# Optimization experiments

Hardware: AMD Instinct MI355X
Metric: run time of the kernel (lower is better)

Reference implementation:

```python
import jax, jax.numpy as jnp
import numpy as np
from jax import lax

DIM = 1024
BATCH = 16
WIDTH = 2048
DECAY = 0.99


def setup_inputs() -> dict:
    key = jax.random.key(0)
    k1, k2, k3, k4 = jax.random.split(key, 4)
    scale = 1.0 / np.sqrt(DIM)
    x = jax.random.normal(k1, (BATCH, WIDTH, DIM), dtype=jnp.float32)
    state = jnp.zeros((BATCH, DIM), dtype=jnp.float32)
    Wv = jax.random.normal(k2, (DIM, DIM), dtype=jnp.float32) * scale
    Wr = jax.random.normal(k3, (DIM, DIM), dtype=jnp.float32) * scale
    Wc = jax.random.normal(k4, (DIM, DIM), dtype=jnp.float32) * scale
    return {"x": x, "state": state, "Wv": Wv, "Wr": Wr, "Wc": Wc}


def reference(x, state, Wv, Wr, Wc):
    # x: [B, W, D], state: [B, D]; fixed-decay RWKV recurrence along width.
    decay = jnp.asarray(DECAY, dtype=x.dtype)
    one_minus = jnp.asarray(1.0, dtype=x.dtype) - decay
    v = jnp.einsum('bwd,de->bwe', x, Wv)                 # value projection
    r = jax.nn.sigmoid(jnp.einsum('bwd,de->bwe', x, Wr))  # receptance

    # scan over width (time) axis: elems shaped [W, B, D]
    def step(s_prev, inp):
        v_t, r_t, x_t = inp
        s_curr = decay * s_prev + one_minus * v_t
        y_t = x_t + r_t * s_curr
        return s_curr, y_t

    elems = (jnp.swapaxes(v, 0, 1), jnp.swapaxes(r, 0, 1), jnp.swapaxes(x, 0, 1))
    new_state, y_t = lax.scan(step, state, elems)
    y = jnp.swapaxes(y_t, 0, 1)                          # [B, W, D]
    y = y + jnp.einsum('bwd,de->bwe', y, Wc)             # minimal channel mix
    return y, new_state
```

## Files before the change

kernel.cpp:

```cpp
#include <hip/hip_runtime.h>
#include <hip/hip_bf16.h>
#include <math.h>


#define MROWS 32768
#define NCHUNK 16
#define CHUNKL 128
#define DECAY_F 0.99f
#define OM_F 0.01f

typedef __attribute__((ext_vector_type(8))) short short8;
typedef __attribute__((ext_vector_type(4))) float floatx4;

using bf16 = __hip_bfloat16;
using bf162 = __hip_bfloat162;

__device__ __forceinline__ void async_copy16(const void* g, void* l) {
  __builtin_amdgcn_global_load_lds(
      (const __attribute__((address_space(1))) unsigned int*)g,
      (__attribute__((address_space(3))) unsigned int*)l, 16, 0, 0);
}

#define S_BARRIER() asm volatile("s_barrier" ::: "memory")
#define VMCNT3()                                                               \
  do {                                                                         \
    asm volatile("s_waitcnt vmcnt(3)" ::: "memory");                           \
    __builtin_amdgcn_sched_barrier(0);                                         \
  } while (0)
#define VMCNT0()                                                               \
  do {                                                                         \
    asm volatile("s_waitcnt vmcnt(0)" ::: "memory");                           \
    __builtin_amdgcn_sched_barrier(0);                                         \
  } while (0)

__global__ void prep_x(const float* __restrict__ X, bf16* __restrict__ Xb) {
  const int idx = blockIdx.x * 256 + threadIdx.x;
  const float4 v = ((const float4*)X)[idx];
  union { ushort4 u; bf16 h[4]; } pk;
  pk.h[0] = __float2bfloat16(v.x);
  pk.h[1] = __float2bfloat16(v.y);
  pk.h[2] = __float2bfloat16(v.z);
  pk.h[3] = __float2bfloat16(v.w);
  ((ushort4*)Xb)[idx] = pk.u;
}

__global__ void prep_weights(const float* __restrict__ Wv,
                             const float* __restrict__ Wr,
                             const float* __restrict__ Wc,
                             bf16* __restrict__ WT) {
  __shared__ float tile[32][33];
  const int bk = blockIdx.x * 32;
  const int bn = blockIdx.y * 32;
  const float* src;
  int nbase = bn;
  if (bn < 1024)      { src = Wv; }
  else if (bn < 2048) { src = Wr; nbase = bn - 1024; }
  else                { src = Wc; nbase = bn - 2048; }
  const int tx = threadIdx.x;
  const int ty = threadIdx.y;
  #pragma unroll
  for (int i = ty; i < 32; i += 8)
    tile[i][tx] = src[(size_t)(bk + i) * 1024 + nbase + tx];
  __syncthreads();
  #pragma unroll
  for (int i = ty; i < 32; i += 8)
    WT[(size_t)(bn + i) * 1024 + bk + tx] = __float2bfloat16(tile[tx][i]);
}

#define PH_MFMA(M0)                                                            \
  __builtin_amdgcn_s_setprio(1);                                               \
  _Pragma("unroll")                                                            \
  for (int nf = 0; nf < 4; ++nf)                                               \
    acc[M0][nf] = __builtin_amdgcn_mfma_f32_16x16x32_bf16(                     \
        fa[M0], fb[nf], acc[M0][nf], 0, 0, 0);                                 \
  _Pragma("unroll")                                                            \
  for (int nf = 0; nf < 4; ++nf)                                               \
    acc[M0 + 1][nf] = __builtin_amdgcn_mfma_f32_16x16x32_bf16(                 \
        fa[M0 + 1], fb[nf], acc[M0 + 1][nf], 0, 0, 0);                         \
  __builtin_amdgcn_s_setprio(0);

#define MFMA_ALL()                                                             \
  __builtin_amdgcn_s_setprio(1);                                               \
  _Pragma("unroll")                                                            \
  for (int mf = 0; mf < 8; ++mf)                                               \
    _Pragma("unroll")                                                          \
    for (int nf = 0; nf < 4; ++nf)                                             \
      acc[mf][nf] = __builtin_amdgcn_mfma_f32_16x16x32_bf16(                   \
          fa[mf], fb[nf], acc[mf][nf], 0, 0, 0);                               \
  __builtin_amdgcn_s_setprio(0);

template <int MODE>
__global__ __launch_bounds__(512, 2) void gemm8(const bf16* __restrict__ Ab,
                                                const bf16* __restrict__ Bw,
                                                bf16* __restrict__ Vout,
                                                bf16* __restrict__ Rout,
                                                float* __restrict__ Fout) {
  __shared__ char lds[65536];
  constexpr int NTN = (MODE == 0) ? 8 : 4;

  const int nwg = gridDim.x;
  const int id = blockIdx.x;
  const int wg = (id & 7) * (nwg >> 3) + (id >> 3);
  const int mt = wg / NTN, nt = wg % NTN;
  const int m0 = mt * 256, n0 = nt * 256;

  const int t = threadIdx.x;
  const int l = t & 63, w = t >> 6;
  const int wm = w >> 2, wn = w & 3;

  const int srow = w * 16 + (l >> 2);
  const int scol = ((l & 3) ^ ((l >> 3) & 3)) << 4;
  const char* Abase = (const char*)Ab;
  const char* Bbase = (const char*)Bw;
  const char* gA0 = Abase + (size_t)(m0 + srow) * 2048 + scol;
  const char* gA1 = gA0 + (size_t)128 * 2048;
  const char* gB0 = Bbase + (size_t)(n0 + srow) * 2048 + scol;
  const char* gB1 = gB0 + (size_t)128 * 2048;

  const int wb = w * 1024;

  const int ll = l & 15;
  const int laneoff = ((ll * 64) + ((l >> 4) << 4)) ^ (((ll >> 1) & 3) << 4);

  floatx4 acc[8][4];
  #pragma unroll
  for (int i = 0; i < 8; ++i)
    #pragma unroll
    for (int j = 0; j < 4; ++j) acc[i][j] = (floatx4){0.f, 0.f, 0.f, 0.f};

  async_copy16(gB0, lds + 16384 + wb);
  async_copy16(gB1, lds + 24576 + wb);
  async_copy16(gA0, lds + 0 + wb);
  async_copy16(gA1, lds + 8192 + wb);
  async_copy16(gB0 + 64, lds + 32768 + 16384 + wb);
  async_copy16(gB1 + 64, lds + 32768 + 24576 + wb);
  async_copy16(gA0 + 64, lds + 32768 + 0 + wb);
  gB0 += 128; gB1 += 128; gA0 += 128; gA1 += 64;
  VMCNT3();
  S_BARRIER();

  short8 fa[8], fb[4];

  for (int T = 0; T < 30; ++T) {
    const int cb = (T & 1) << 15;
    const char* smA = lds + cb + wm * 8192 + laneoff;
    const char* smB = lds + cb + 16384 + wn * 4096 + laneoff;
    #pragma unroll
    for (int nf = 0; nf < 4; ++nf) fb[nf] = *(const short8*)(smB + nf * 1024);
    #pragma unroll
    for (int mf = 0; mf < 4; ++mf) fa[mf] = *(const short8*)(smA + mf * 1024);
    async_copy16(gA1, lds + (cb ^ 32768) + 8192 + wb); gA1 += 64;
    S_BARRIER();
    PH_MFMA(0)
    S_BARRIER();
    #pragma unroll
    for (int mf = 4; mf < 8; ++mf) fa[mf] = *(const short8*)(smA + mf * 1024);
    async_copy16(gB0, lds + cb + 16384 + wb); gB0 += 64;
    S_BARRIER();
    PH_MFMA(2)
    S_BARRIER();
    async_copy16(gB1, lds + cb + 24576 + wb); gB1 += 64;
    S_BARRIER();
    PH_MFMA(4)
    S_BARRIER();
    async_copy16(gA0, lds + cb + wb); gA0 += 64;
    S_BARRIER();
    PH_MFMA(6)
    VMCNT3();
    S_BARRIER();
  }

  {
    const char* smA = lds + wm * 8192 + laneoff;
    const char* smB = lds + 16384 + wn * 4096 + laneoff;
    #pragma unroll
    for (int nf = 0; nf < 4; ++nf) fb[nf] = *(const short8*)(smB + nf * 1024);
    #pragma unroll
    for (int mf = 0; mf < 8; ++mf) fa[mf] = *(const short8*)(smA + mf * 1024);
    async_copy16(gA1, lds + 32768 + 8192 + wb);
    MFMA_ALL()
    VMCNT0();
    S_BARRIER();
  }
  {
    const char* smA = lds + 32768 + wm * 8192 + laneoff;
    const char* smB = lds + 32768 + 16384 + wn * 4096 + laneoff;
    #pragma unroll
    for (int nf = 0; nf < 4; ++nf) fb[nf] = *(const short8*)(smB + nf * 1024);
    #pragma unroll
    for (int mf = 0; mf < 8; ++mf) fa[mf] = *(const short8*)(smA + mf * 1024);
    MFMA_ALL()
  }

  const int orow0 = m0 + wm * 128 + (l >> 4) * 4;
  const int ocol = n0 + wn * 64 + ll;
  if constexpr (MODE == 0) {
    const bool isr = (n0 >= 1024);
    bf16* outp = isr ? Rout : Vout;
    const int oc = isr ? (ocol - 1024) : ocol;
    #pragma unroll
    for (int mf = 0; mf < 8; ++mf) {
      #pragma unroll
      for (int i = 0; i < 4; ++i) {
        const size_t ro = (size_t)(orow0 + mf * 16 + i) * 1024 + oc;
        #pragma unroll
        for (int nf = 0; nf < 4; ++nf) {
          float cv = acc[mf][nf][i];
          if (isr) cv = 1.0f / (1.0f + __expf(-cv));
          outp[ro + nf * 16] = __float2bfloat16(cv);
        }
      }
    }
  } else {
    #pragma unroll
    for (int mf = 0; mf < 8; ++mf) {
      #pragma unroll
      for (int i = 0; i < 4; ++i) {
        const size_t ro = (size_t)(orow0 + mf * 16 + i) * 1024 + ocol;
        #pragma unroll
        for (int nf = 0; nf < 4; ++nf) {
          const size_t o = ro + nf * 16;
          Fout[o] = __bfloat162float(Ab[o]) + acc[mf][nf][i];
        }
      }
    }
  }
}

__global__ void scan_partial(const bf16* __restrict__ V, float* __restrict__ sl) {
  const int idx = blockIdx.x * 256 + threadIdx.x;
  const int d2 = idx & 511;
  const int c = (idx >> 9) & 15;
  const int b = idx >> 13;
  const bf162* V2 = (const bf162*)V;
  const size_t base = (size_t)(b * 2048 + c * 128) * 512 + d2;
  float s0 = 0.f, s1 = 0.f;
  for (int w = 0; w < CHUNKL; ++w) {
    const bf162 v = V2[base + (size_t)w * 512];
    s0 = DECAY_F * s0 + OM_F * __bfloat162float(v.x);
    s1 = DECAY_F * s1 + OM_F * __bfloat162float(v.y);
  }
  const int o = (b * 16 + c) * 1024 + d2 * 2;
  sl[o] = s0;
  sl[o + 1] = s1;
}

__global__ void scan_chunk(const float* __restrict__ state,
                           const float* __restrict__ sl,
                           float* __restrict__ sin_,
                           float* __restrict__ state_out,
                           float decayL) {
  const int idx = blockIdx.x * 256 + threadIdx.x;
  const int d = idx & 1023;
  const int b = idx >> 10;
  float s = state[idx];
  #pragma unroll
  for (int c = 0; c < NCHUNK; ++c) {
    const int o = (b * 16 + c) * 1024 + d;
    sin_[o] = s;
    s = decayL * s + sl[o];
  }
  state_out[idx] = s;
}

__global__ void scan_apply(const bf16* __restrict__ Xb,
                           const bf16* __restrict__ R,
                           const float* __restrict__ sin_,
                           bf16* __restrict__ VY) {
  const int idx = blockIdx.x * 256 + threadIdx.x;
  const int d2 = idx & 511;
  const int c = (idx >> 9) & 15;
  const int b = idx >> 13;
  const bf162* R2 = (const bf162*)R;
  const bf162* X2 = (const bf162*)Xb;
  bf162* VY2 = (bf162*)VY;
  const size_t base = (size_t)(b * 2048 + c * 128) * 512 + d2;
  const int so = (b * 16 + c) * 1024 + d2 * 2;
  float s0 = sin_[so], s1 = sin_[so + 1];
  for (int w = 0; w < CHUNKL; ++w) {
    const size_t off = base + (size_t)w * 512;
    const bf162 v = VY2[off];
    const bf162 r = R2[off];
    const bf162 xx = X2[off];
    s0 = DECAY_F * s0 + OM_F * __bfloat162float(v.x);
    s1 = DECAY_F * s1 + OM_F * __bfloat162float(v.y);
    const float y0 = __bfloat162float(xx.x) + __bfloat162float(r.x) * s0;
    const float y1 = __bfloat162float(xx.y) + __bfloat162float(r.y) * s1;
    bf162 o;
    o.x = __float2bfloat16(y0);
    o.y = __float2bfloat16(y1);
    VY2[off] = o;
  }
}

extern "C" void kernel_launch(void* const* d_in, const int* in_sizes, int n_in,
                              void* d_out, int out_size, void* d_ws, size_t ws_size,
                              hipStream_t stream) {
  const float* x     = (const float*)d_in[0];
  const float* state = (const float*)d_in[1];
  const float* Wv    = (const float*)d_in[2];
  const float* Wr    = (const float*)d_in[3];
  const float* Wc    = (const float*)d_in[4];

  float* y_out = (float*)d_out;
  float* state_out = y_out + (size_t)MROWS * 1024;

  char* ws = (char*)d_ws;
  bf16* WT   = (bf16*)ws;
  bf16* Xb   = (bf16*)(ws + ((size_t)6 << 20));
  bf16* Vbuf = (bf16*)(ws + ((size_t)70 << 20));
  bf16* Rbuf = (bf16*)(ws + ((size_t)134 << 20));
  float* sl  = (float*)(ws + ((size_t)198 << 20));
  float* sin_ = (float*)(ws + ((size_t)199 << 20));
  bf16* WcT = WT + (size_t)2048 * 1024;

  const float decayL = (float)pow(0.99, (double)CHUNKL);

  prep_x<<<32768, 256, 0, stream>>>(x, Xb);
  prep_weights<<<dim3(32, 96), dim3(32, 8), 0, stream>>>(Wv, Wr, Wc, WT);
  gemm8<0><<<1024, 512, 0, stream>>>(Xb, WT, Vbuf, Rbuf, nullptr);
  scan_partial<<<512, 256, 0, stream>>>(Vbuf, sl);
  scan_chunk<<<64, 256, 0, stream>>>(state, sl, sin_, state_out, decayL);
  scan_apply<<<512, 256, 0, stream>>>(Xb, Rbuf, sin_, Vbuf);
  gemm8<1><<<512, 512, 0, stream>>>(Vbuf, WcT, nullptr, nullptr, y_out);
}
```

Measured before the change: 515.4 us.

## Restructure GEMM main loop into two phases with fewer barriers

Reworks the software pipeline of the bf16 MFMA GEMM. Each iteration now issues both A-tile prefetches for the next buffer up front, loads all A and B fragments at once, and runs two 16-MFMA phases separated by a single barrier, with the B refills issued in between. The previous loop had eight barriers around four 8-MFMA phases. The prologue and tail are reordered to match, and the wait count drops to vmcnt(2). Fewer barriers should cut synchronisation stalls, at the cost of more fragment registers live at once and coarser interleaving of loads with MFMAs.

```diff
diff --git a/kernel.cpp b/kernel.cpp
--- a/kernel.cpp
+++ b/kernel.cpp
@@ -22,9 +22,9 @@
 }
 
 #define S_BARRIER() asm volatile("s_barrier" ::: "memory")
-#define VMCNT3()                                                               \
+#define VMCNT2()                                                               \
   do {                                                                         \
-    asm volatile("s_waitcnt vmcnt(3)" ::: "memory");                           \
+    asm volatile("s_waitcnt vmcnt(2)" ::: "memory");                           \
     __builtin_amdgcn_sched_barrier(0);                                         \
   } while (0)
 #define VMCNT0()                                                               \
@@ -67,16 +67,14 @@
     WT[(size_t)(bn + i) * 1024 + bk + tx] = __float2bfloat16(tile[tx][i]);
 }
 
-#define PH_MFMA(M0)                                                            \
+#define PH_MFMA4(M0)                                                           \
   __builtin_amdgcn_s_setprio(1);                                               \
   _Pragma("unroll")                                                            \
-  for (int nf = 0; nf < 4; ++nf)                                               \
-    acc[M0][nf] = __builtin_amdgcn_mfma_f32_16x16x32_bf16(                     \
-        fa[M0], fb[nf], acc[M0][nf], 0, 0, 0);                                 \
-  _Pragma("unroll")                                                            \
-  for (int nf = 0; nf < 4; ++nf)                                               \
-    acc[M0 + 1][nf] = __builtin_amdgcn_mfma_f32_16x16x32_bf16(                 \
-        fa[M0 + 1], fb[nf], acc[M0 + 1][nf], 0, 0, 0);                         \
+  for (int mf = M0; mf < M0 + 4; ++mf)                                         \
+    _Pragma("unroll")                                                          \
+    for (int nf = 0; nf < 4; ++nf)                                             \
+      acc[mf][nf] = __builtin_amdgcn_mfma_f32_16x16x32_bf16(                   \
+          fa[mf], fb[nf], acc[mf][nf], 0, 0, 0);                               \
   __builtin_amdgcn_s_setprio(0);
 
 #define MFMA_ALL()                                                             \
@@ -128,15 +126,14 @@
     #pragma unroll
     for (int j = 0; j < 4; ++j) acc[i][j] = (floatx4){0.f, 0.f, 0.f, 0.f};
 
+  async_copy16(gA0, lds + 0 + wb);
+  async_copy16(gA1, lds + 8192 + wb);
   async_copy16(gB0, lds + 16384 + wb);
   async_copy16(gB1, lds + 24576 + wb);
-  async_copy16(gA0, lds + 0 + wb);
-  async_copy16(gA1, lds + 8192 + wb);
   async_copy16(gB0 + 64, lds + 32768 + 16384 + wb);
   async_copy16(gB1 + 64, lds + 32768 + 24576 + wb);
-  async_copy16(gA0 + 64, lds + 32768 + 0 + wb);
-  gB0 += 128; gB1 += 128; gA0 += 128; gA1 += 64;
-  VMCNT3();
+  gA0 += 64; gA1 += 64; gB0 += 128; gB1 += 128;
+  VMCNT2();
   S_BARRIER();
 
   short8 fa[8], fb[4];
@@ -145,28 +142,18 @@
     const int cb = (T & 1) << 15;
     const char* smA = lds + cb + wm * 8192 + laneoff;
     const char* smB = lds + cb + 16384 + wn * 4096 + laneoff;
+    async_copy16(gA0, lds + (cb ^ 32768) + 0 + wb); gA0 += 64;
+    async_copy16(gA1, lds + (cb ^ 32768) + 8192 + wb); gA1 += 64;
     #pragma unroll
     for (int nf = 0; nf < 4; ++nf) fb[nf] = *(const short8*)(smB + nf * 1024);
     #pragma unroll
-    for (int mf = 0; mf < 4; ++mf) fa[mf] = *(const short8*)(smA + mf * 1024);
-    async_copy16(gA1, lds + (cb ^ 32768) + 8192 + wb); gA1 += 64;
+    for (int mf = 0; mf < 8; ++mf) fa[mf] = *(const short8*)(smA + mf * 1024);
+    PH_MFMA4(0)
     S_BARRIER();
-    PH_MFMA(0)
-    S_BARRIER();
-    #pragma unroll
-    for (int mf = 4; mf < 8; ++mf) fa[mf] = *(const short8*)(smA + mf * 1024);
     async_copy16(gB0, lds + cb + 16384 + wb); gB0 += 64;
-    S_BARRIER();
-    PH_MFMA(2)
-    S_BARRIER();
     async_copy16(gB1, lds + cb + 24576 + wb); gB1 += 64;
-    S_BARRIER();
-    PH_MFMA(4)
-    S_BARRIER();
-    async_copy16(gA0, lds + cb + wb); gA0 += 64;
-    S_BARRIER();
-    PH_MFMA(6)
-    VMCNT3();
+    PH_MFMA4(4)
+    VMCNT2();
     S_BARRIER();
   }
 
@@ -177,6 +164,7 @@
     for (int nf = 0; nf < 4; ++nf) fb[nf] = *(const short8*)(smB + nf * 1024);
     #pragma unroll
     for (int mf = 0; mf < 8; ++mf) fa[mf] = *(const short8*)(smA + mf * 1024);
+    async_copy16(gA0, lds + 32768 + 0 + wb);
     async_copy16(gA1, lds + 32768 + 8192 + wb);
     MFMA_ALL()
     VMCNT0();
```

Result: no change. 507.0 us (-1.6%).
